# Kernel optimization log

Hardware: AMD Instinct MI355X
Metric: run time of the kernel (lower is better)

Reference implementation:

```python
import jax, jax.numpy as jnp
import numpy as np

EPS = 1e-12  # F.normalize default eps


def setup_inputs() -> dict:
    key = jax.random.key(0)
    k1, k2 = jax.random.split(key)
    E, N, B, T, Fdim, K = 2, 512, 64, 12, 2, 64
    supports = jax.random.uniform(k1, (E, N, N), dtype=jnp.float32)
    inputs = jax.random.normal(k2, (B, T, N, Fdim), dtype=jnp.float32)
    bias = jnp.ones((E, K), dtype=jnp.float32)  # init.ones_
    # torch.svd at __init__: A = u @ diag(s) @ v^T, truncated to node_dim
    u_np, s_np, vh_np = np.linalg.svd(np.asarray(supports), full_matrices=False)
    u = jnp.asarray(u_np[..., :K])                      # [E, N, K]
    s = jnp.asarray(s_np[..., :K])                      # [E, K]
    v = jnp.asarray(np.swapaxes(vh_np, -1, -2)[..., :K])  # [E, N, K]
    return {"supports": supports, "u": u, "s": s, "v": v, "bias": bias, "inputs": inputs}


def _pairwise_dist(x):
    # x: [B, N, T] L2-normalized rows; returns [B, N, N] Euclidean distances
    sq = jnp.sum(x * x, axis=-1)                      # [B, N]
    inner = jnp.einsum('bnt,bmt->bnm', x, x)          # [B, N, N]
    d2 = jnp.maximum(sq[:, :, None] + sq[:, None, :] - 2.0 * inner, 0.0)
    # safe sqrt (zero on the diagonal, matching torch.cdist)
    pos = d2 > 0
    return jnp.where(pos, jnp.sqrt(jnp.where(pos, d2, 1.0)), 0.0)


def reference(supports, u, s, v, bias, inputs):
    # SAdaptor: low-rank SVD reconstruction with softplus-scaled singular values
    s_scaled = s * jax.nn.softplus(bias)              # [E, K]
    adaptive = jnp.einsum('enk,ek,emk->enm', u, s_scaled, v)  # [E, N, N]
    sup = supports + adaptive                         # [E, N, N]

    # TAdaptor: exp(-cdist) of L2-normalized node histories (dropout: eval mode)
    x = jnp.transpose(inputs[..., 0], (0, 2, 1))      # [B, N, T]
    nrm = jnp.sqrt(jnp.sum(x * x, axis=-1, keepdims=True))
    nodes = x / jnp.maximum(nrm, EPS)                 # F.normalize(p=2)
    dynamic = jnp.exp(-_pairwise_dist(nodes))         # [B, N, N]

    out = sup[:, None, :, :] * (dynamic[None] + 1.0)  # [E, B, N, N]
    out = jax.nn.relu(out)
    # F.normalize(p=1, dim=-1); out >= 0 so |out| == out
    return out / jnp.maximum(jnp.sum(out, axis=-1, keepdims=True), EPS)
```

## Files before the change

### kernel.cpp

```cpp
#include <hip/hip_runtime.h>

#define E 2
#define N 512
#define B 64
#define T 12
#define K 64
#define NB 4

template<int CTRL, int RM>
__device__ __forceinline__ float dpp_add(float x) {
    int y = __builtin_amdgcn_update_dpp(0, __float_as_int(x), CTRL, RM, 0xf, true);
    return x + __int_as_float(y);
}
__device__ __forceinline__ float wave_sum64(float x) {
    x = dpp_add<0x111, 0xf>(x);
    x = dpp_add<0x112, 0xf>(x);
    x = dpp_add<0x114, 0xf>(x);
    x = dpp_add<0x118, 0xf>(x);
    x = dpp_add<0x142, 0xa>(x);
    x = dpp_add<0x143, 0xc>(x);
    return __int_as_float(__builtin_amdgcn_readlane(__float_as_int(x), 63));
}

__global__ __launch_bounds__(512)
void k_prep(const float* __restrict__ supports, const float* __restrict__ uu,
            const float* __restrict__ ss, const float* __restrict__ vv,
            const float* __restrict__ bias, const float* __restrict__ inp,
            float* __restrict__ sup, float* __restrict__ nodes) {
    const int blk = blockIdx.x;
    const int tid = threadIdx.x;
    if (blk < 2 * (N / NB)) {
        const int e = blk >> 7;
        const int n0 = (blk & 127) * NB;
        __shared__ float uls[NB][K];
        if (tid < NB * K) {
            const int j = tid >> 6, k = tid & 63;
            float bb = bias[e * K + k];
            float sp_ = (bb > 0.f) ? (bb + log1pf(expf(-bb))) : log1pf(expf(bb));
            uls[j][k] = uu[(size_t)(e * N + n0 + j) * K + k] * ss[e * K + k] * sp_;
        }
        __syncthreads();
        const int m = tid;
        const float4* vp = reinterpret_cast<const float4*>(vv + (size_t)(e * N + m) * K);
        float accs[NB] = {0.f, 0.f, 0.f, 0.f};
#pragma unroll
        for (int i = 0; i < 16; ++i) {
            float4 q = vp[i];
#pragma unroll
            for (int j = 0; j < NB; ++j) {
                const float* w = &uls[j][i * 4];
                accs[j] += w[0] * q.x + w[1] * q.y + w[2] * q.z + w[3] * q.w;
            }
        }
#pragma unroll
        for (int j = 0; j < NB; ++j) {
            const size_t o = (size_t)(e * N + n0 + j) * N + m;
            sup[o] = accs[j] + supports[o];
        }
    } else {
        const int idx = (blk - 2 * (N / NB)) * 512 + tid;
        const int b = idx >> 9, n = idx & (N - 1);
        float x[T];
        float sq = 0.f;
#pragma unroll
        for (int t = 0; t < T; ++t) {
            float xv = inp[((size_t)(b * T + t) * N + n) * 2];
            x[t] = xv;
            sq += xv * xv;
        }
        float inv = 1.f / fmaxf(sqrtf(sq), 1e-12f);
#pragma unroll
        for (int t = 0; t < T; ++t) nodes[(size_t)idx * T + t] = x[t] * inv;
    }
}

__global__ __launch_bounds__(512)
void k_main(const float* __restrict__ sup, const float* __restrict__ nodes,
            float* __restrict__ out) {
    const int bi = blockIdx.x;
    const int b = bi >> 7;
    const int n0 = (bi & 127) * NB;
    const int t = threadIdx.x;
    const int g = __builtin_amdgcn_readfirstlane(t >> 7);
    const int m0 = (t & 127) * 4;
    const int wave = t >> 6, lane = t & 63;

    __shared__ float red[8][2];

    const float* __restrict__ anc = nodes + ((size_t)(b * N) + n0 + g) * T;
    float a[T];
#pragma unroll
    for (int i = 0; i < T; ++i) a[i] = anc[i];

    const float4* np4 = reinterpret_cast<const float4*>(nodes + ((size_t)(b * N) + m0) * T);
    float4 nr[12];
#pragma unroll
    for (int i = 0; i < 12; ++i) nr[i] = np4[i];
    const float* x = reinterpret_cast<const float*>(nr);

    float4 s0 = *reinterpret_cast<const float4*>(sup + (size_t)(n0 + g) * N + m0);
    float4 s1 = *reinterpret_cast<const float4*>(sup + (size_t)N * N + (size_t)(n0 + g) * N + m0);
    const float* sp0 = reinterpret_cast<const float*>(&s0);
    const float* sp1 = reinterpret_cast<const float*>(&s1);

    float v0[4], v1[4];
    float ls0 = 0.f, ls1 = 0.f;
#pragma unroll
    for (int k = 0; k < 4; ++k) {
        float d2 = 0.f;
#pragma unroll
        for (int i = 0; i < T; ++i) {
            float d = x[k * T + i] - a[i];
            d2 += d * d;
        }
        float dist = (d2 > 0.f) ? sqrtf(d2) : 0.f;
        float f = __expf(-dist) + 1.f;
        v0[k] = fmaxf(sp0[k] * f, 0.f);
        v1[k] = fmaxf(sp1[k] * f, 0.f);
        ls0 += v0[k];
        ls1 += v1[k];
    }

    float w0 = wave_sum64(ls0);
    float w1 = wave_sum64(ls1);
    if (lane == 0) { red[wave][0] = w0; red[wave][1] = w1; }
    __syncthreads();

    float inv0 = 1.f / fmaxf(red[2 * g][0] + red[2 * g + 1][0], 1e-12f);
    float inv1 = 1.f / fmaxf(red[2 * g][1] + red[2 * g + 1][1], 1e-12f);

    float4 o0 = make_float4(v0[0] * inv0, v0[1] * inv0, v0[2] * inv0, v0[3] * inv0);
    float4 o1 = make_float4(v1[0] * inv1, v1[1] * inv1, v1[2] * inv1, v1[3] * inv1);
    *reinterpret_cast<float4*>(out + ((size_t)(0 * B + b) * N + n0 + g) * N + m0) = o0;
    *reinterpret_cast<float4*>(out + ((size_t)(1 * B + b) * N + n0 + g) * N + m0) = o1;
}

extern "C" void kernel_launch(void* const* d_in, const int* in_sizes, int n_in,
                              void* d_out, int out_size, void* d_ws, size_t ws_size,
                              hipStream_t stream) {
    const float* supports = (const float*)d_in[0];
    const float* uu       = (const float*)d_in[1];
    const float* ss       = (const float*)d_in[2];
    const float* vv       = (const float*)d_in[3];
    const float* bias     = (const float*)d_in[4];
    const float* inp      = (const float*)d_in[5];
    float* out = (float*)d_out;

    float* sup   = (float*)d_ws;
    float* nodes = sup + (size_t)E * N * N;

    k_prep<<<2 * (N / NB) + (B * N) / 512, 512, 0, stream>>>(
        supports, uu, ss, vv, bias, inp, sup, nodes);
    k_main<<<B * (N / NB), 512, 0, stream>>>(sup, nodes, out);
}
```

Measured before the change: 190.0 us.

## Tile main kernel by wave-owned rows with transposed node cache and dot-based distance

Each wave now owns 8 output rows across the full 512 columns. Each lane keeps 8 columns of node vectors in registers and reuses them across those rows, so the block-level shared-memory reduction and barrier are replaced by wave-only reductions. Prep also writes a transposed copy of the nodes so these column loads are coalesced. Distance is computed as 2-2*dot, which assumes unit-norm rows; this drops subtractions but can differ slightly for zero-norm rows or from rounding.

```diff
diff --git a/kernel.cpp b/kernel.cpp
--- a/kernel.cpp
+++ b/kernel.cpp
@@ -5,7 +5,8 @@
 #define B 64
 #define T 12
 #define K 64
-#define NB 4
+#define NBR 8
+#define RPB 32
 
 template<int CTRL, int RM>
 __device__ __forceinline__ float dpp_add(float x) {
@@ -26,14 +27,14 @@
 void k_prep(const float* __restrict__ supports, const float* __restrict__ uu,
             const float* __restrict__ ss, const float* __restrict__ vv,
             const float* __restrict__ bias, const float* __restrict__ inp,
-            float* __restrict__ sup, float* __restrict__ nodes) {
-    const int blk = blockIdx.x;
-    const int tid = threadIdx.x;
-    if (blk < 2 * (N / NB)) {
+            float* __restrict__ sup, float* __restrict__ nodes,
+            float* __restrict__ nodesT) {
+    const int blk = blockIdx.x, tid = threadIdx.x;
+    if (blk < 256) {
         const int e = blk >> 7;
-        const int n0 = (blk & 127) * NB;
-        __shared__ float uls[NB][K];
-        if (tid < NB * K) {
+        const int n0 = (blk & 127) * 4;
+        __shared__ float uls[4][K];
+        if (tid < 4 * K) {
             const int j = tid >> 6, k = tid & 63;
             float bb = bias[e * K + k];
             float sp_ = (bb > 0.f) ? (bb + log1pf(expf(-bb))) : log1pf(expf(bb));
@@ -42,24 +43,24 @@
         __syncthreads();
         const int m = tid;
         const float4* vp = reinterpret_cast<const float4*>(vv + (size_t)(e * N + m) * K);
-        float accs[NB] = {0.f, 0.f, 0.f, 0.f};
+        float accs[4] = {0.f, 0.f, 0.f, 0.f};
 #pragma unroll
         for (int i = 0; i < 16; ++i) {
             float4 q = vp[i];
 #pragma unroll
-            for (int j = 0; j < NB; ++j) {
+            for (int j = 0; j < 4; ++j) {
                 const float* w = &uls[j][i * 4];
                 accs[j] += w[0] * q.x + w[1] * q.y + w[2] * q.z + w[3] * q.w;
             }
         }
 #pragma unroll
-        for (int j = 0; j < NB; ++j) {
+        for (int j = 0; j < 4; ++j) {
             const size_t o = (size_t)(e * N + n0 + j) * N + m;
             sup[o] = accs[j] + supports[o];
         }
     } else {
-        const int idx = (blk - 2 * (N / NB)) * 512 + tid;
-        const int b = idx >> 9, n = idx & (N - 1);
+        const int b = blk - 256;
+        const int n = tid;
         float x[T];
         float sq = 0.f;
 #pragma unroll
@@ -70,69 +71,81 @@
         }
         float inv = 1.f / fmaxf(sqrtf(sq), 1e-12f);
 #pragma unroll
-        for (int t = 0; t < T; ++t) nodes[(size_t)idx * T + t] = x[t] * inv;
+        for (int t = 0; t < T; ++t) {
+            float xv = x[t] * inv;
+            nodes[((size_t)(b * N) + n) * T + t] = xv;
+            nodesT[((size_t)(b * T) + t) * N + n] = xv;
+        }
     }
 }
 
-__global__ __launch_bounds__(512)
+__global__ __launch_bounds__(256)
 void k_main(const float* __restrict__ sup, const float* __restrict__ nodes,
-            float* __restrict__ out) {
+            const float* __restrict__ nodesT, float* __restrict__ out) {
     const int bi = blockIdx.x;
-    const int b = bi >> 7;
-    const int n0 = (bi & 127) * NB;
-    const int t = threadIdx.x;
-    const int g = __builtin_amdgcn_readfirstlane(t >> 7);
-    const int m0 = (t & 127) * 4;
-    const int wave = t >> 6, lane = t & 63;
+    const int b = bi >> 4;
+    const int wave = __builtin_amdgcn_readfirstlane((int)threadIdx.x >> 6);
+    const int lane = threadIdx.x & 63;
+    const int n0 = (bi & 15) * RPB + wave * NBR;
+    const int m0 = lane * 8;
 
-    __shared__ float red[8][2];
-
-    const float* __restrict__ anc = nodes + ((size_t)(b * N) + n0 + g) * T;
-    float a[T];
+    float x[T][8];
 #pragma unroll
-    for (int i = 0; i < T; ++i) a[i] = anc[i];
-
-    const float4* np4 = reinterpret_cast<const float4*>(nodes + ((size_t)(b * N) + m0) * T);
-    float4 nr[12];
-#pragma unroll
-    for (int i = 0; i < 12; ++i) nr[i] = np4[i];
-    const float* x = reinterpret_cast<const float*>(nr);
-
-    float4 s0 = *reinterpret_cast<const float4*>(sup + (size_t)(n0 + g) * N + m0);
-    float4 s1 = *reinterpret_cast<const float4*>(sup + (size_t)N * N + (size_t)(n0 + g) * N + m0);
-    const float* sp0 = reinterpret_cast<const float*>(&s0);
-    const float* sp1 = reinterpret_cast<const float*>(&s1);
-
-    float v0[4], v1[4];
-    float ls0 = 0.f, ls1 = 0.f;
-#pragma unroll
-    for (int k = 0; k < 4; ++k) {
-        float d2 = 0.f;
-#pragma unroll
-        for (int i = 0; i < T; ++i) {
-            float d = x[k * T + i] - a[i];
-            d2 += d * d;
-        }
-        float dist = (d2 > 0.f) ? sqrtf(d2) : 0.f;
-        float f = __expf(-dist) + 1.f;
-        v0[k] = fmaxf(sp0[k] * f, 0.f);
-        v1[k] = fmaxf(sp1[k] * f, 0.f);
-        ls0 += v0[k];
-        ls1 += v1[k];
+    for (int t = 0; t < T; ++t) {
+        const float* cp = nodesT + ((size_t)(b * T) + t) * N + m0;
+        float4 c0 = *reinterpret_cast<const float4*>(cp);
+        float4 c1 = *reinterpret_cast<const float4*>(cp + 4);
+        x[t][0] = c0.x; x[t][1] = c0.y; x[t][2] = c0.z; x[t][3] = c0.w;
+        x[t][4] = c1.x; x[t][5] = c1.y; x[t][6] = c1.z; x[t][7] = c1.w;
     }
 
-    float w0 = wave_sum64(ls0);
-    float w1 = wave_sum64(ls1);
-    if (lane == 0) { red[wave][0] = w0; red[wave][1] = w1; }
-    __syncthreads();
+#pragma unroll
+    for (int j = 0; j < NBR; ++j) {
+        const int n = n0 + j;
+        const float* ap = nodes + ((size_t)(b * N) + n) * T;
+        float4 a0 = *reinterpret_cast<const float4*>(ap);
+        float4 a1 = *reinterpret_cast<const float4*>(ap + 4);
+        float4 a2 = *reinterpret_cast<const float4*>(ap + 8);
+        float a[T] = {a0.x, a0.y, a0.z, a0.w, a1.x, a1.y, a1.z, a1.w,
+                      a2.x, a2.y, a2.z, a2.w};
 
-    float inv0 = 1.f / fmaxf(red[2 * g][0] + red[2 * g + 1][0], 1e-12f);
-    float inv1 = 1.f / fmaxf(red[2 * g][1] + red[2 * g + 1][1], 1e-12f);
+        const float* s0p = sup + (size_t)n * N + m0;
+        const float* s1p = s0p + (size_t)N * N;
+        float4 sA = *reinterpret_cast<const float4*>(s0p);
+        float4 sB = *reinterpret_cast<const float4*>(s0p + 4);
+        float4 sC = *reinterpret_cast<const float4*>(s1p);
+        float4 sD = *reinterpret_cast<const float4*>(s1p + 4);
+        float sp0[8] = {sA.x, sA.y, sA.z, sA.w, sB.x, sB.y, sB.z, sB.w};
+        float sp1[8] = {sC.x, sC.y, sC.z, sC.w, sD.x, sD.y, sD.z, sD.w};
 
-    float4 o0 = make_float4(v0[0] * inv0, v0[1] * inv0, v0[2] * inv0, v0[3] * inv0);
-    float4 o1 = make_float4(v1[0] * inv1, v1[1] * inv1, v1[2] * inv1, v1[3] * inv1);
-    *reinterpret_cast<float4*>(out + ((size_t)(0 * B + b) * N + n0 + g) * N + m0) = o0;
-    *reinterpret_cast<float4*>(out + ((size_t)(1 * B + b) * N + n0 + g) * N + m0) = o1;
+        float v0[8], v1[8];
+        float p0 = 0.f, p1 = 0.f;
+#pragma unroll
+        for (int k = 0; k < 8; ++k) {
+            float dot = 0.f;
+#pragma unroll
+            for (int t = 0; t < T; ++t) dot = fmaf(x[t][k], a[t], dot);
+            float d2 = fmaxf(2.f - 2.f * dot, 0.f);
+            float f = __expf(-sqrtf(d2)) + 1.f;
+            v0[k] = fmaxf(sp0[k] * f, 0.f);
+            v1[k] = fmaxf(sp1[k] * f, 0.f);
+            p0 += v0[k];
+            p1 += v1[k];
+        }
+        float inv0 = 1.f / fmaxf(wave_sum64(p0), 1e-12f);
+        float inv1 = 1.f / fmaxf(wave_sum64(p1), 1e-12f);
+
+        float* o0 = out + ((size_t)(b * N) + n) * N + m0;
+        float* o1 = o0 + (size_t)B * N * N;
+        *reinterpret_cast<float4*>(o0) =
+            make_float4(v0[0] * inv0, v0[1] * inv0, v0[2] * inv0, v0[3] * inv0);
+        *reinterpret_cast<float4*>(o0 + 4) =
+            make_float4(v0[4] * inv0, v0[5] * inv0, v0[6] * inv0, v0[7] * inv0);
+        *reinterpret_cast<float4*>(o1) =
+            make_float4(v1[0] * inv1, v1[1] * inv1, v1[2] * inv1, v1[3] * inv1);
+        *reinterpret_cast<float4*>(o1 + 4) =
+            make_float4(v1[4] * inv1, v1[5] * inv1, v1[6] * inv1, v1[7] * inv1);
+    }
 }
 
 extern "C" void kernel_launch(void* const* d_in, const int* in_sizes, int n_in,
@@ -146,10 +159,11 @@
     const float* inp      = (const float*)d_in[5];
     float* out = (float*)d_out;
 
-    float* sup   = (float*)d_ws;
-    float* nodes = sup + (size_t)E * N * N;
+    float* sup    = (float*)d_ws;
+    float* nodes  = sup + (size_t)E * N * N;
+    float* nodesT = nodes + (size_t)B * N * T;
 
-    k_prep<<<2 * (N / NB) + (B * N) / 512, 512, 0, stream>>>(
-        supports, uu, ss, vv, bias, inp, sup, nodes);
-    k_main<<<B * (N / NB), 512, 0, stream>>>(sup, nodes, out);
+    k_prep<<<256 + B, 512, 0, stream>>>(supports, uu, ss, vv, bias, inp,
+                                        sup, nodes, nodesT);
+    k_main<<<B * (N / RPB), 256, 0, stream>>>(sup, nodes, nodesT, out);
 }
```

After: 167.8 us. -11.6%, faster.
